# Performance work log

Hardware: AMD Instinct MI355X
Metric: run time of the kernel (lower is better)

The kernel has to match this reference:

```python
import jax, jax.numpy as jnp
import numpy as np

H = 1024
E = 8
TOP_K = 2
B, S = 4, 2048


def setup_inputs() -> dict:
    key = jax.random.key(0)
    ks = jax.random.split(key, 8)
    scale = 0.02
    return {
        "x": jax.random.normal(ks[0], (B, S, H), dtype=jnp.float32),
        "router_w": jax.random.normal(ks[1], (H, E), dtype=jnp.float32) * scale,
        "router_b": jnp.zeros((E,), dtype=jnp.float32),
        "w1": jax.random.normal(ks[2], (E, H, 4 * H), dtype=jnp.float32) * scale,
        "b1": jnp.zeros((E, 4 * H), dtype=jnp.float32),
        "w2": jax.random.normal(ks[3], (E, 4 * H, H), dtype=jnp.float32) * scale,
        "b2": jnp.zeros((E, H), dtype=jnp.float32),
    }


def reference(x, router_w, router_b, w1, b1, w2, b2):
    b, s, h = x.shape
    n_exp = w1.shape[0]
    x_flat = x.reshape(-1, h)  # [T, H]
    T = x_flat.shape[0]

    # Router: softmax then top-k, renormalize top-k probs (matches torch code).
    logits = x_flat @ router_w + router_b            # [T, E]
    probs = jax.nn.softmax(logits, axis=-1)
    top_values, top_indices = jax.lax.top_k(probs, TOP_K)  # [T, k]
    top_values = top_values / jnp.sum(top_values, axis=-1, keepdims=True)

    # Per-token combine weight for each expert (0 if token not routed there).
    combine = jnp.zeros((T, n_exp), dtype=x.dtype)
    combine = combine.at[jnp.arange(T)[:, None], top_indices].add(top_values)  # [T, E]

    # Loop over the small fixed expert set; masked combine weights zero out
    # contributions from unrouted tokens, matching the gather/scatter original.
    out = jnp.zeros_like(x_flat)
    for e in range(n_exp):
        hmid = jax.nn.gelu(x_flat @ w1[e] + b1[e], approximate=False)  # [T, 4H]
        y = hmid @ w2[e] + b2[e]                                       # [T, H]
        out = out + combine[:, e:e + 1] * y
    return out.reshape(b, s, h)
```

## Files before the change

kernel.cpp:

```cpp
#include <hip/hip_runtime.h>
#include <hip/hip_bf16.h>
#include <math.h>

#define TT 8192
#define HD 1024
#define FHD 4096
#define NE 8
#define NTMAX 136

typedef short s16x8 __attribute__((ext_vector_type(8)));
typedef float f32x4 __attribute__((ext_vector_type(4)));
using bf16 = __hip_bfloat16;
typedef unsigned int u32;

#define OFF_COUNTS 0
#define OFF_CURSOR 64
#define OFF_OFFS   128
#define OFF_E0     256
#define OFF_E1     (OFF_E0 + 4*TT)
#define OFF_W0     (OFF_E1 + 4*TT)
#define OFF_W1     (OFF_W0 + 4*TT)
#define OFF_S0     (OFF_W1 + 4*TT)
#define OFF_S1     (OFF_S0 + 4*TT)
#define OFF_TID    (OFF_S1 + 4*TT)
#define OFF_TW     (OFF_TID + 8*TT)
#define OFF_TMR    (OFF_TW + 8*TT)
#define OFF_TME    (OFF_TMR + 4*144)
#define OFF_TMN    (OFF_TME + 4*144)
#define OFF_XBF    (OFF_TMN + 64)
#define OFF_W1T    (OFF_XBF + 2*TT*HD)
#define OFF_W2T    (OFF_W1T + 2*NE*HD*FHD)
#define OFF_HMID   (OFF_W2T + 2*NE*HD*FHD)
#define OFF_YS     (OFF_HMID + (size_t)2*(2*TT)*FHD)

#define BM 128
#define BN 128
#define BK 32

__device__ __forceinline__ void gload_lds16(const void* g, void* l) {
    __builtin_amdgcn_global_load_lds(
        (const __attribute__((address_space(1))) u32*)g,
        (__attribute__((address_space(3))) u32*)l, 16, 0, 0);
}

__global__ __launch_bounds__(256) void cast_x_kernel(const float* __restrict__ x, bf16* __restrict__ xbf) {
    int i = (blockIdx.x * 256 + threadIdx.x) * 8;
    float4 a = *reinterpret_cast<const float4*>(&x[i]);
    float4 b = *reinterpret_cast<const float4*>(&x[i + 4]);
    bf16 h[8];
    h[0] = __float2bfloat16(a.x); h[1] = __float2bfloat16(a.y);
    h[2] = __float2bfloat16(a.z); h[3] = __float2bfloat16(a.w);
    h[4] = __float2bfloat16(b.x); h[5] = __float2bfloat16(b.y);
    h[6] = __float2bfloat16(b.z); h[7] = __float2bfloat16(b.w);
    *reinterpret_cast<uint4*>(&xbf[i]) = *reinterpret_cast<uint4*>(h);
}

__global__ __launch_bounds__(256) void transpose_cast_kernel(const float* __restrict__ in,
        bf16* __restrict__ out, int R, int C) {
    __shared__ float tile[64][65];
    int rt = R >> 6, ct = C >> 6;
    int e = blockIdx.x / (rt * ct);
    int rem = blockIdx.x % (rt * ct);
    int r0 = (rem / ct) << 6, c0 = (rem % ct) << 6;
    const float* ine = in + (size_t)e * R * C;
    bf16* oute = out + (size_t)e * R * C;
    int tid = threadIdx.x;
#pragma unroll
    for (int i = 0; i < 4; ++i) {
        int lin = tid + i * 256;
        int r = lin >> 4, cg = lin & 15;
        float4 v = *reinterpret_cast<const float4*>(&ine[(size_t)(r0 + r) * C + c0 + cg * 4]);
        tile[r][cg * 4 + 0] = v.x; tile[r][cg * 4 + 1] = v.y;
        tile[r][cg * 4 + 2] = v.z; tile[r][cg * 4 + 3] = v.w;
    }
    __syncthreads();
#pragma unroll
    for (int i = 0; i < 4; ++i) {
        int lin = tid + i * 256;
        int n = lin >> 4, kg = lin & 15;
        bf16 h[4];
        h[0] = __float2bfloat16(tile[kg * 4 + 0][n]);
        h[1] = __float2bfloat16(tile[kg * 4 + 1][n]);
        h[2] = __float2bfloat16(tile[kg * 4 + 2][n]);
        h[3] = __float2bfloat16(tile[kg * 4 + 3][n]);
        *reinterpret_cast<uint2*>(&oute[(size_t)(c0 + n) * R + r0 + kg * 4]) =
            *reinterpret_cast<uint2*>(h);
    }
}

__global__ __launch_bounds__(256) void router_kernel(const float* __restrict__ x,
        const float* __restrict__ rw, const float* __restrict__ rb,
        int* __restrict__ e0a, int* __restrict__ e1a,
        float* __restrict__ w0a, float* __restrict__ w1a, int* __restrict__ counts) {
    int wid = threadIdx.x >> 6, lane = threadIdx.x & 63;
    int t = blockIdx.x * 4 + wid;
    const float* xp = x + (size_t)t * HD + lane * 16;
    float xv[16];
#pragma unroll
    for (int j = 0; j < 4; ++j) {
        float4 v = *reinterpret_cast<const float4*>(&xp[j * 4]);
        xv[4 * j] = v.x; xv[4 * j + 1] = v.y; xv[4 * j + 2] = v.z; xv[4 * j + 3] = v.w;
    }
    float acc[8] = {0.f, 0.f, 0.f, 0.f, 0.f, 0.f, 0.f, 0.f};
    const float* rp = rw + (size_t)(lane * 16) * NE;
#pragma unroll
    for (int hh = 0; hh < 16; ++hh) {
        float4 r0 = *reinterpret_cast<const float4*>(&rp[hh * 8]);
        float4 r1 = *reinterpret_cast<const float4*>(&rp[hh * 8 + 4]);
        acc[0] += xv[hh] * r0.x; acc[1] += xv[hh] * r0.y;
        acc[2] += xv[hh] * r0.z; acc[3] += xv[hh] * r0.w;
        acc[4] += xv[hh] * r1.x; acc[5] += xv[hh] * r1.y;
        acc[6] += xv[hh] * r1.z; acc[7] += xv[hh] * r1.w;
    }
#pragma unroll
    for (int e = 0; e < 8; ++e) {
#pragma unroll
        for (int off = 32; off > 0; off >>= 1) acc[e] += __shfl_xor(acc[e], off, 64);
    }
    if (lane == 0) {
        float lg[8];
#pragma unroll
        for (int e = 0; e < 8; ++e) lg[e] = acc[e] + rb[e];
        int a = 0;
#pragma unroll
        for (int e = 1; e < 8; ++e) if (lg[e] > lg[a]) a = e;
        int b = (a == 0) ? 1 : 0;
#pragma unroll
        for (int e = 0; e < 8; ++e) if (e != a && e != b && lg[e] > lg[b]) b = e;
        float wa = 1.0f / (1.0f + expf(lg[b] - lg[a]));
        float wb = 1.0f / (1.0f + expf(lg[a] - lg[b]));
        e0a[t] = a; e1a[t] = b; w0a[t] = wa; w1a[t] = wb;
        atomicAdd(&counts[a], 1);
        atomicAdd(&counts[b], 1);
    }
}

__global__ void scan_offsets_kernel(const int* __restrict__ counts, int* __restrict__ offs,
        int* __restrict__ cursor, int* __restrict__ tmr, int* __restrict__ tme,
        int* __restrict__ tmn) {
    if (threadIdx.x == 0 && blockIdx.x == 0) {
        int s = 0, nt = 0;
        for (int e = 0; e < NE; ++e) {
            offs[e] = s; cursor[e] = s;
            int c = counts[e];
            for (int j = 0; j < c; j += BM) { tmr[nt] = s + j; tme[nt] = e; ++nt; }
            s += c;
        }
        offs[NE] = s;
        tmn[0] = nt;
        for (int i = nt; i < NTMAX; ++i) { tmr[i] = 0; tme[i] = 0; }
    }
}

__global__ __launch_bounds__(256) void scatter_kernel(const int* __restrict__ e0a, const int* __restrict__ e1a,
        const float* __restrict__ w0a, const float* __restrict__ w1a,
        int* __restrict__ cursor, int* __restrict__ tid_arr, float* __restrict__ tw_arr,
        int* __restrict__ slot0, int* __restrict__ slot1) {
    int t = blockIdx.x * 256 + threadIdx.x;
    int s0 = atomicAdd(&cursor[e0a[t]], 1);
    tid_arr[s0] = t; tw_arr[s0] = w0a[t]; slot0[t] = s0;
    int s1 = atomicAdd(&cursor[e1a[t]], 1);
    tid_arr[s1] = t; tw_arr[s1] = w1a[t]; slot1[t] = s1;
}

__global__ __launch_bounds__(256) void gemm1_kernel(const bf16* __restrict__ xbf, const bf16* __restrict__ w1t,
        const float* __restrict__ b1, const int* __restrict__ offs,
        const int* __restrict__ tid_arr, bf16* __restrict__ hmid,
        const int* __restrict__ tmr, const int* __restrict__ tme, const int* __restrict__ tmn) {
    __shared__ bf16 As[BM * BK];
    __shared__ bf16 Bs[BN * BK];
    __shared__ int toks[BM];
    int nwg = gridDim.x;
    int orig = blockIdx.x;
    int wg = (orig & 7) * (nwg >> 3) + (orig >> 3);
    int nt = wg / NTMAX;
    int tidx = wg % NTMAX;
    if (tidx >= tmn[0]) return;
    int e = tme[tidx];
    int row0 = tmr[tidx];
    int s1 = offs[e + 1];
    int n0 = nt * BN;
    int tid = threadIdx.x;
    if (tid < BM) { int s = row0 + tid; toks[tid] = tid_arr[(s < s1) ? s : (s1 - 1)]; }
    __syncthreads();
    int lane = tid & 63, w = tid >> 6;
    int wrow = (w >> 1) * 64, wcol = (w & 1) * 64;
    int lr = lane & 15, lk = (lane >> 4) * 8;
    int srow = lane >> 2, seg = lane & 3;
    int tokA0 = toks[w * 32 + srow];
    int tokA1 = toks[w * 32 + 16 + srow];
    const bf16* w1e = w1t + (size_t)e * FHD * HD;
    const bf16* bsrc0 = w1e + (size_t)(n0 + w * 32 + srow) * HD + seg * 8;
    const bf16* bsrc1 = w1e + (size_t)(n0 + w * 32 + 16 + srow) * HD + seg * 8;
    const bf16* asrc0 = xbf + (size_t)tokA0 * HD + seg * 8;
    const bf16* asrc1 = xbf + (size_t)tokA1 * HD + seg * 8;
    bf16* aDst0 = &As[(w * 32) * BK];
    bf16* aDst1 = &As[(w * 32 + 16) * BK];
    bf16* bDst0 = &Bs[(w * 32) * BK];
    bf16* bDst1 = &Bs[(w * 32 + 16) * BK];
    f32x4 acc[4][4] = {};
    for (int k0 = 0; k0 < HD; k0 += BK) {
        gload_lds16(asrc0 + k0, aDst0);
        gload_lds16(asrc1 + k0, aDst1);
        gload_lds16(bsrc0 + k0, bDst0);
        gload_lds16(bsrc1 + k0, bDst1);
        __syncthreads();
        s16x8 aF[4], bF[4];
#pragma unroll
        for (int m = 0; m < 4; ++m) aF[m] = *reinterpret_cast<const s16x8*>(&As[(wrow + m * 16 + lr) * BK + lk]);
#pragma unroll
        for (int n = 0; n < 4; ++n) bF[n] = *reinterpret_cast<const s16x8*>(&Bs[(wcol + n * 16 + lr) * BK + lk]);
#pragma unroll
        for (int m = 0; m < 4; ++m)
#pragma unroll
            for (int n = 0; n < 4; ++n)
                acc[m][n] = __builtin_amdgcn_mfma_f32_16x16x32_bf16(aF[m], bF[n], acc[m][n], 0, 0, 0);
        __syncthreads();
    }
#pragma unroll
    for (int m = 0; m < 4; ++m) {
#pragma unroll
        for (int n = 0; n < 4; ++n) {
            int col = n0 + wcol + n * 16 + lr;
            float bv = b1[(size_t)e * FHD + col];
#pragma unroll
            for (int r = 0; r < 4; ++r) {
                int row = wrow + m * 16 + (lane >> 4) * 4 + r;
                int slot = row0 + row;
                if (slot < s1) {
                    float v2 = acc[m][n][r] + bv;
                    v2 = 0.5f * v2 * (1.0f + erff(v2 * 0.70710678118f));
                    hmid[(size_t)slot * FHD + col] = __float2bfloat16(v2);
                }
            }
        }
    }
}

__global__ __launch_bounds__(256) void gemm2_kernel(const bf16* __restrict__ hmid, const bf16* __restrict__ w2t,
        const float* __restrict__ b2, const int* __restrict__ offs, float* __restrict__ ys,
        const int* __restrict__ tmr, const int* __restrict__ tme, const int* __restrict__ tmn) {
    __shared__ bf16 As[BM * BK];
    __shared__ bf16 Bs[BN * BK];
    int nwg = gridDim.x;
    int orig = blockIdx.x;
    int wg = (orig & 7) * (nwg >> 3) + (orig >> 3);
    int nt = wg / NTMAX;
    int tidx = wg % NTMAX;
    if (tidx >= tmn[0]) return;
    int e = tme[tidx];
    int row0 = tmr[tidx];
    int s1 = offs[e + 1];
    int n0 = nt * BN;
    int tid = threadIdx.x;
    int lane = tid & 63, w = tid >> 6;
    int wrow = (w >> 1) * 64, wcol = (w & 1) * 64;
    int lr = lane & 15, lk = (lane >> 4) * 8;
    int srow = lane >> 2, seg = lane & 3;
    int ar0 = row0 + w * 32 + srow;      if (ar0 >= s1) ar0 = s1 - 1;
    int ar1 = row0 + w * 32 + 16 + srow; if (ar1 >= s1) ar1 = s1 - 1;
    const bf16* w2e = w2t + (size_t)e * HD * FHD;
    const bf16* bsrc0 = w2e + (size_t)(n0 + w * 32 + srow) * FHD + seg * 8;
    const bf16* bsrc1 = w2e + (size_t)(n0 + w * 32 + 16 + srow) * FHD + seg * 8;
    const bf16* asrc0 = hmid + (size_t)ar0 * FHD + seg * 8;
    const bf16* asrc1 = hmid + (size_t)ar1 * FHD + seg * 8;
    bf16* aDst0 = &As[(w * 32) * BK];
    bf16* aDst1 = &As[(w * 32 + 16) * BK];
    bf16* bDst0 = &Bs[(w * 32) * BK];
    bf16* bDst1 = &Bs[(w * 32 + 16) * BK];
    f32x4 acc[4][4] = {};
    for (int k0 = 0; k0 < FHD; k0 += BK) {
        gload_lds16(asrc0 + k0, aDst0);
        gload_lds16(asrc1 + k0, aDst1);
        gload_lds16(bsrc0 + k0, bDst0);
        gload_lds16(bsrc1 + k0, bDst1);
        __syncthreads();
        s16x8 aF[4], bF[4];
#pragma unroll
        for (int m = 0; m < 4; ++m) aF[m] = *reinterpret_cast<const s16x8*>(&As[(wrow + m * 16 + lr) * BK + lk]);
#pragma unroll
        for (int n = 0; n < 4; ++n) bF[n] = *reinterpret_cast<const s16x8*>(&Bs[(wcol + n * 16 + lr) * BK + lk]);
#pragma unroll
        for (int m = 0; m < 4; ++m)
#pragma unroll
            for (int n = 0; n < 4; ++n)
                acc[m][n] = __builtin_amdgcn_mfma_f32_16x16x32_bf16(aF[m], bF[n], acc[m][n], 0, 0, 0);
        __syncthreads();
    }
#pragma unroll
    for (int m = 0; m < 4; ++m) {
#pragma unroll
        for (int n = 0; n < 4; ++n) {
            int col = n0 + wcol + n * 16 + lr;
            float bv = b2[(size_t)e * HD + col];
#pragma unroll
            for (int r = 0; r < 4; ++r) {
                int row = wrow + m * 16 + (lane >> 4) * 4 + r;
                int slot = row0 + row;
                if (slot < s1) ys[(size_t)slot * HD + col] = acc[m][n][r] + bv;
            }
        }
    }
}

__global__ __launch_bounds__(256) void combine_kernel(const float* __restrict__ ys,
        const int* __restrict__ slot0, const int* __restrict__ slot1,
        const float* __restrict__ tw, float* __restrict__ out) {
    int t = blockIdx.x;
    int c = threadIdx.x * 4;
    int sa = slot0[t], sb = slot1[t];
    float wa = tw[sa], wb = tw[sb];
    float4 a = *reinterpret_cast<const float4*>(&ys[(size_t)sa * HD + c]);
    float4 b = *reinterpret_cast<const float4*>(&ys[(size_t)sb * HD + c]);
    float4 o;
    o.x = wa * a.x + wb * b.x; o.y = wa * a.y + wb * b.y;
    o.z = wa * a.z + wb * b.z; o.w = wa * a.w + wb * b.w;
    *reinterpret_cast<float4*>(&out[(size_t)t * HD + c]) = o;
}

extern "C" void kernel_launch(void* const* d_in, const int* in_sizes, int n_in,
                              void* d_out, int out_size, void* d_ws, size_t ws_size,
                              hipStream_t stream) {
    const float* x  = (const float*)d_in[0];
    const float* rw = (const float*)d_in[1];
    const float* rb = (const float*)d_in[2];
    const float* w1 = (const float*)d_in[3];
    const float* b1 = (const float*)d_in[4];
    const float* w2 = (const float*)d_in[5];
    const float* b2 = (const float*)d_in[6];
    float* out = (float*)d_out;
    char* ws = (char*)d_ws;

    int*   counts  = (int*)(ws + OFF_COUNTS);
    int*   cursor  = (int*)(ws + OFF_CURSOR);
    int*   offs    = (int*)(ws + OFF_OFFS);
    int*   e0a     = (int*)(ws + OFF_E0);
    int*   e1a     = (int*)(ws + OFF_E1);
    float* w0a     = (float*)(ws + OFF_W0);
    float* w1a     = (float*)(ws + OFF_W1);
    int*   slot0   = (int*)(ws + OFF_S0);
    int*   slot1   = (int*)(ws + OFF_S1);
    int*   tid_arr = (int*)(ws + OFF_TID);
    float* tw_arr  = (float*)(ws + OFF_TW);
    int*   tmr     = (int*)(ws + OFF_TMR);
    int*   tme     = (int*)(ws + OFF_TME);
    int*   tmn     = (int*)(ws + OFF_TMN);
    bf16*  xbf     = (bf16*)(ws + OFF_XBF);
    bf16*  w1t     = (bf16*)(ws + OFF_W1T);
    bf16*  w2t     = (bf16*)(ws + OFF_W2T);
    bf16*  hmid    = (bf16*)(ws + OFF_HMID);
    float* ys      = (float*)(ws + OFF_YS);

    hipMemsetAsync(counts, 0, 64, stream);

    cast_x_kernel<<<TT * HD / 2048, 256, 0, stream>>>(x, xbf);
    transpose_cast_kernel<<<NE * (HD / 64) * (FHD / 64), 256, 0, stream>>>(w1, w1t, HD, FHD);
    transpose_cast_kernel<<<NE * (FHD / 64) * (HD / 64), 256, 0, stream>>>(w2, w2t, FHD, HD);
    router_kernel<<<TT / 4, 256, 0, stream>>>(x, rw, rb, e0a, e1a, w0a, w1a, counts);
    scan_offsets_kernel<<<1, 64, 0, stream>>>(counts, offs, cursor, tmr, tme, tmn);
    scatter_kernel<<<TT / 256, 256, 0, stream>>>(e0a, e1a, w0a, w1a, cursor, tid_arr, tw_arr, slot0, slot1);
    gemm1_kernel<<<(FHD / BN) * NTMAX, 256, 0, stream>>>(xbf, w1t, b1, offs, tid_arr, hmid, tmr, tme, tmn);
    gemm2_kernel<<<(HD / BN) * NTMAX, 256, 0, stream>>>(hmid, w2t, b2, offs, ys, tmr, tme, tmn);
    combine_kernel<<<TT, 256, 0, stream>>>(ys, slot0, slot1, tw_arr, out);
}
```

Before: 929.2 us.

## Fuse weight transpose, x cast, router and offset scan into one prep kernel

Merges the x cast, both weight transpose-casts, the router, and the offset/tile-map scan into a single prep kernel. The x bf16 cast is folded into the router's existing x read, and the last router block (found with a done-counter atomic) builds offsets and the tile map in parallel. The aim is to remove several kernel launches and a redundant read of x. The BM/BN/BK macros are also inlined as literals. The done counter sits inside the 64-byte region that is memset each call, so it is reset correctly. The fused scan relies on threadfence and atomic ordering.

```diff
diff --git a/kernel.cpp b/kernel.cpp
--- a/kernel.cpp
+++ b/kernel.cpp
@@ -14,6 +14,7 @@
 typedef unsigned int u32;
 
 #define OFF_COUNTS 0
+#define OFF_DONE   32
 #define OFF_CURSOR 64
 #define OFF_OFFS   128
 #define OFF_E0     256
@@ -33,73 +34,74 @@
 #define OFF_HMID   (OFF_W2T + 2*NE*HD*FHD)
 #define OFF_YS     (OFF_HMID + (size_t)2*(2*TT)*FHD)
 
-#define BM 128
-#define BN 128
-#define BK 32
-
 __device__ __forceinline__ void gload_lds16(const void* g, void* l) {
     __builtin_amdgcn_global_load_lds(
         (const __attribute__((address_space(1))) u32*)g,
         (__attribute__((address_space(3))) u32*)l, 16, 0, 0);
 }
 
-__global__ __launch_bounds__(256) void cast_x_kernel(const float* __restrict__ x, bf16* __restrict__ xbf) {
-    int i = (blockIdx.x * 256 + threadIdx.x) * 8;
-    float4 a = *reinterpret_cast<const float4*>(&x[i]);
-    float4 b = *reinterpret_cast<const float4*>(&x[i + 4]);
-    bf16 h[8];
-    h[0] = __float2bfloat16(a.x); h[1] = __float2bfloat16(a.y);
-    h[2] = __float2bfloat16(a.z); h[3] = __float2bfloat16(a.w);
-    h[4] = __float2bfloat16(b.x); h[5] = __float2bfloat16(b.y);
-    h[6] = __float2bfloat16(b.z); h[7] = __float2bfloat16(b.w);
-    *reinterpret_cast<uint4*>(&xbf[i]) = *reinterpret_cast<uint4*>(h);
-}
-
-__global__ __launch_bounds__(256) void transpose_cast_kernel(const float* __restrict__ in,
-        bf16* __restrict__ out, int R, int C) {
+__global__ __launch_bounds__(256) void prep_kernel(
+        const float* __restrict__ x, const float* __restrict__ rw, const float* __restrict__ rb,
+        const float* __restrict__ w1, const float* __restrict__ w2,
+        bf16* __restrict__ xbf, bf16* __restrict__ w1t, bf16* __restrict__ w2t,
+        int* __restrict__ e0a, int* __restrict__ e1a,
+        float* __restrict__ w0a, float* __restrict__ w1a,
+        int* __restrict__ counts, int* __restrict__ done,
+        int* __restrict__ offs, int* __restrict__ cursor,
+        int* __restrict__ tmr, int* __restrict__ tme, int* __restrict__ tmn) {
     __shared__ float tile[64][65];
-    int rt = R >> 6, ct = C >> 6;
-    int e = blockIdx.x / (rt * ct);
-    int rem = blockIdx.x % (rt * ct);
-    int r0 = (rem / ct) << 6, c0 = (rem % ct) << 6;
-    const float* ine = in + (size_t)e * R * C;
-    bf16* oute = out + (size_t)e * R * C;
+    int bid = blockIdx.x;
     int tid = threadIdx.x;
-#pragma unroll
-    for (int i = 0; i < 4; ++i) {
-        int lin = tid + i * 256;
-        int r = lin >> 4, cg = lin & 15;
-        float4 v = *reinterpret_cast<const float4*>(&ine[(size_t)(r0 + r) * C + c0 + cg * 4]);
-        tile[r][cg * 4 + 0] = v.x; tile[r][cg * 4 + 1] = v.y;
-        tile[r][cg * 4 + 2] = v.z; tile[r][cg * 4 + 3] = v.w;
-    }
-    __syncthreads();
-#pragma unroll
-    for (int i = 0; i < 4; ++i) {
-        int lin = tid + i * 256;
-        int n = lin >> 4, kg = lin & 15;
-        bf16 h[4];
-        h[0] = __float2bfloat16(tile[kg * 4 + 0][n]);
-        h[1] = __float2bfloat16(tile[kg * 4 + 1][n]);
-        h[2] = __float2bfloat16(tile[kg * 4 + 2][n]);
-        h[3] = __float2bfloat16(tile[kg * 4 + 3][n]);
-        *reinterpret_cast<uint2*>(&oute[(size_t)(c0 + n) * R + r0 + kg * 4]) =
-            *reinterpret_cast<uint2*>(h);
-    }
-}
-
-__global__ __launch_bounds__(256) void router_kernel(const float* __restrict__ x,
-        const float* __restrict__ rw, const float* __restrict__ rb,
-        int* __restrict__ e0a, int* __restrict__ e1a,
-        float* __restrict__ w0a, float* __restrict__ w1a, int* __restrict__ counts) {
-    int wid = threadIdx.x >> 6, lane = threadIdx.x & 63;
-    int t = blockIdx.x * 4 + wid;
+    if (bid < 16384) {
+        const float* in; bf16* out; int R, C, rem;
+        if (bid < 8192) { in = w1; out = w1t; R = HD;  C = FHD; rem = bid; }
+        else            { in = w2; out = w2t; R = FHD; C = HD;  rem = bid - 8192; }
+        int rt = R >> 6, ct = C >> 6;
+        int e = rem / (rt * ct);
+        int rem2 = rem % (rt * ct);
+        int r0 = (rem2 / ct) << 6, c0 = (rem2 % ct) << 6;
+        const float* ine = in + (size_t)e * R * C;
+        bf16* oute = out + (size_t)e * R * C;
+#pragma unroll
+        for (int i = 0; i < 4; ++i) {
+            int lin = tid + i * 256;
+            int r = lin >> 4, cg = lin & 15;
+            float4 v = *reinterpret_cast<const float4*>(&ine[(size_t)(r0 + r) * C + c0 + cg * 4]);
+            tile[r][cg * 4 + 0] = v.x; tile[r][cg * 4 + 1] = v.y;
+            tile[r][cg * 4 + 2] = v.z; tile[r][cg * 4 + 3] = v.w;
+        }
+        __syncthreads();
+#pragma unroll
+        for (int i = 0; i < 4; ++i) {
+            int lin = tid + i * 256;
+            int n = lin >> 4, kg = lin & 15;
+            bf16 h[4];
+            h[0] = __float2bfloat16(tile[kg * 4 + 0][n]);
+            h[1] = __float2bfloat16(tile[kg * 4 + 1][n]);
+            h[2] = __float2bfloat16(tile[kg * 4 + 2][n]);
+            h[3] = __float2bfloat16(tile[kg * 4 + 3][n]);
+            *reinterpret_cast<uint2*>(&oute[(size_t)(c0 + n) * R + r0 + kg * 4]) =
+                *reinterpret_cast<uint2*>(h);
+        }
+        return;
+    }
+    int rbid = bid - 16384;
+    int wid = tid >> 6, lane = tid & 63;
+    int t = rbid * 4 + wid;
     const float* xp = x + (size_t)t * HD + lane * 16;
     float xv[16];
 #pragma unroll
     for (int j = 0; j < 4; ++j) {
         float4 v = *reinterpret_cast<const float4*>(&xp[j * 4]);
         xv[4 * j] = v.x; xv[4 * j + 1] = v.y; xv[4 * j + 2] = v.z; xv[4 * j + 3] = v.w;
+    }
+    {
+        bf16 hv[16];
+#pragma unroll
+        for (int j = 0; j < 16; ++j) hv[j] = __float2bfloat16(xv[j]);
+        uint4* dst = reinterpret_cast<uint4*>(&xbf[(size_t)t * HD + lane * 16]);
+        dst[0] = reinterpret_cast<uint4*>(hv)[0];
+        dst[1] = reinterpret_cast<uint4*>(hv)[1];
     }
     float acc[8] = {0.f, 0.f, 0.f, 0.f, 0.f, 0.f, 0.f, 0.f};
     const float* rp = rw + (size_t)(lane * 16) * NE;
@@ -133,22 +135,37 @@
         atomicAdd(&counts[a], 1);
         atomicAdd(&counts[b], 1);
     }
-}
-
-__global__ void scan_offsets_kernel(const int* __restrict__ counts, int* __restrict__ offs,
-        int* __restrict__ cursor, int* __restrict__ tmr, int* __restrict__ tme,
-        int* __restrict__ tmn) {
-    if (threadIdx.x == 0 && blockIdx.x == 0) {
-        int s = 0, nt = 0;
+    __syncthreads();
+    __shared__ int lastFlag;
+    if (tid == 0) {
+        __threadfence();
+        lastFlag = (atomicAdd(done, 1) == 2047) ? 1 : 0;
+    }
+    __syncthreads();
+    if (!lastFlag) return;
+    __threadfence();
+    __shared__ int cbase[NE + 1], tbase[NE + 1];
+    if (tid == 0) {
+        int s = 0, ntt = 0;
         for (int e = 0; e < NE; ++e) {
-            offs[e] = s; cursor[e] = s;
-            int c = counts[e];
-            for (int j = 0; j < c; j += BM) { tmr[nt] = s + j; tme[nt] = e; ++nt; }
-            s += c;
-        }
+            int c = atomicAdd(&counts[e], 0);
+            cbase[e] = s; tbase[e] = ntt;
+            s += c; ntt += (c + 127) >> 7;
+        }
+        cbase[NE] = s; tbase[NE] = ntt;
+        tmn[0] = ntt;
         offs[NE] = s;
-        tmn[0] = nt;
-        for (int i = nt; i < NTMAX; ++i) { tmr[i] = 0; tme[i] = 0; }
+    }
+    __syncthreads();
+    if (tid < NE) { offs[tid] = cbase[tid]; cursor[tid] = cbase[tid]; }
+    if (tid < NTMAX) {
+        int ntt = tbase[NE];
+        if (tid < ntt) {
+            int e = 0;
+            while (tbase[e + 1] <= tid) ++e;
+            tmr[tid] = cbase[e] + ((tid - tbase[e]) << 7);
+            tme[tid] = e;
+        } else { tmr[tid] = 0; tme[tid] = 0; }
     }
 }
 
@@ -167,9 +184,9 @@
         const float* __restrict__ b1, const int* __restrict__ offs,
         const int* __restrict__ tid_arr, bf16* __restrict__ hmid,
         const int* __restrict__ tmr, const int* __restrict__ tme, const int* __restrict__ tmn) {
-    __shared__ bf16 As[BM * BK];
-    __shared__ bf16 Bs[BN * BK];
-    __shared__ int toks[BM];
+    __shared__ bf16 As[128 * 32];
+    __shared__ bf16 Bs[128 * 32];
+    __shared__ int toks[128];
     int nwg = gridDim.x;
     int orig = blockIdx.x;
     int wg = (orig & 7) * (nwg >> 3) + (orig >> 3);
@@ -179,9 +196,9 @@
     int e = tme[tidx];
     int row0 = tmr[tidx];
     int s1 = offs[e + 1];
-    int n0 = nt * BN;
+    int n0 = nt * 128;
     int tid = threadIdx.x;
-    if (tid < BM) { int s = row0 + tid; toks[tid] = tid_arr[(s < s1) ? s : (s1 - 1)]; }
+    if (tid < 128) { int s = row0 + tid; toks[tid] = tid_arr[(s < s1) ? s : (s1 - 1)]; }
     __syncthreads();
     int lane = tid & 63, w = tid >> 6;
     int wrow = (w >> 1) * 64, wcol = (w & 1) * 64;
@@ -194,12 +211,12 @@
     const bf16* bsrc1 = w1e + (size_t)(n0 + w * 32 + 16 + srow) * HD + seg * 8;
     const bf16* asrc0 = xbf + (size_t)tokA0 * HD + seg * 8;
     const bf16* asrc1 = xbf + (size_t)tokA1 * HD + seg * 8;
-    bf16* aDst0 = &As[(w * 32) * BK];
-    bf16* aDst1 = &As[(w * 32 + 16) * BK];
-    bf16* bDst0 = &Bs[(w * 32) * BK];
-    bf16* bDst1 = &Bs[(w * 32 + 16) * BK];
+    bf16* aDst0 = &As[(w * 32) * 32];
+    bf16* aDst1 = &As[(w * 32 + 16) * 32];
+    bf16* bDst0 = &Bs[(w * 32) * 32];
+    bf16* bDst1 = &Bs[(w * 32 + 16) * 32];
     f32x4 acc[4][4] = {};
-    for (int k0 = 0; k0 < HD; k0 += BK) {
+    for (int k0 = 0; k0 < HD; k0 += 32) {
         gload_lds16(asrc0 + k0, aDst0);
         gload_lds16(asrc1 + k0, aDst1);
         gload_lds16(bsrc0 + k0, bDst0);
@@ -207,9 +224,9 @@
         __syncthreads();
         s16x8 aF[4], bF[4];
 #pragma unroll
-        for (int m = 0; m < 4; ++m) aF[m] = *reinterpret_cast<const s16x8*>(&As[(wrow + m * 16 + lr) * BK + lk]);
-#pragma unroll
-        for (int n = 0; n < 4; ++n) bF[n] = *reinterpret_cast<const s16x8*>(&Bs[(wcol + n * 16 + lr) * BK + lk]);
+        for (int m = 0; m < 4; ++m) aF[m] = *reinterpret_cast<const s16x8*>(&As[(wrow + m * 16 + lr) * 32 + lk]);
+#pragma unroll
+        for (int n = 0; n < 4; ++n) bF[n] = *reinterpret_cast<const s16x8*>(&Bs[(wcol + n * 16 + lr) * 32 + lk]);
 #pragma unroll
         for (int m = 0; m < 4; ++m)
 #pragma unroll
@@ -240,8 +257,8 @@
 __global__ __launch_bounds__(256) void gemm2_kernel(const bf16* __restrict__ hmid, const bf16* __restrict__ w2t,
         const float* __restrict__ b2, const int* __restrict__ offs, float* __restrict__ ys,
         const int* __restrict__ tmr, const int* __restrict__ tme, const int* __restrict__ tmn) {
-    __shared__ bf16 As[BM * BK];
-    __shared__ bf16 Bs[BN * BK];
+    __shared__ bf16 As[128 * 32];
+    __shared__ bf16 Bs[128 * 32];
     int nwg = gridDim.x;
     int orig = blockIdx.x;
     int wg = (orig & 7) * (nwg >> 3) + (orig >> 3);
@@ -251,7 +268,7 @@
     int e = tme[tidx];
     int row0 = tmr[tidx];
     int s1 = offs[e + 1];
-    int n0 = nt * BN;
+    int n0 = nt * 128;
     int tid = threadIdx.x;
     int lane = tid & 63, w = tid >> 6;
     int wrow = (w >> 1) * 64, wcol = (w & 1) * 64;
@@ -264,12 +281,12 @@
     const bf16* bsrc1 = w2e + (size_t)(n0 + w * 32 + 16 + srow) * FHD + seg * 8;
     const bf16* asrc0 = hmid + (size_t)ar0 * FHD + seg * 8;
     const bf16* asrc1 = hmid + (size_t)ar1 * FHD + seg * 8;
-    bf16* aDst0 = &As[(w * 32) * BK];
-    bf16* aDst1 = &As[(w * 32 + 16) * BK];
-    bf16* bDst0 = &Bs[(w * 32) * BK];
-    bf16* bDst1 = &Bs[(w * 32 + 16) * BK];
+    bf16* aDst0 = &As[(w * 32) * 32];
+    bf16* aDst1 = &As[(w * 32 + 16) * 32];
+    bf16* bDst0 = &Bs[(w * 32) * 32];
+    bf16* bDst1 = &Bs[(w * 32 + 16) * 32];
     f32x4 acc[4][4] = {};
-    for (int k0 = 0; k0 < FHD; k0 += BK) {
+    for (int k0 = 0; k0 < FHD; k0 += 32) {
         gload_lds16(asrc0 + k0, aDst0);
         gload_lds16(asrc1 + k0, aDst1);
         gload_lds16(bsrc0 + k0, bDst0);
@@ -277,9 +294,9 @@
         __syncthreads();
         s16x8 aF[4], bF[4];
 #pragma unroll
-        for (int m = 0; m < 4; ++m) aF[m] = *reinterpret_cast<const s16x8*>(&As[(wrow + m * 16 + lr) * BK + lk]);
-#pragma unroll
-        for (int n = 0; n < 4; ++n) bF[n] = *reinterpret_cast<const s16x8*>(&Bs[(wcol + n * 16 + lr) * BK + lk]);
+        for (int m = 0; m < 4; ++m) aF[m] = *reinterpret_cast<const s16x8*>(&As[(wrow + m * 16 + lr) * 32 + lk]);
+#pragma unroll
+        for (int n = 0; n < 4; ++n) bF[n] = *reinterpret_cast<const s16x8*>(&Bs[(wcol + n * 16 + lr) * 32 + lk]);
 #pragma unroll
         for (int m = 0; m < 4; ++m)
 #pragma unroll
@@ -332,6 +349,7 @@
     char* ws = (char*)d_ws;
 
     int*   counts  = (int*)(ws + OFF_COUNTS);
+    int*   done    = (int*)(ws + OFF_DONE);
     int*   cursor  = (int*)(ws + OFF_CURSOR);
     int*   offs    = (int*)(ws + OFF_OFFS);
     int*   e0a     = (int*)(ws + OFF_E0);
@@ -353,13 +371,11 @@
 
     hipMemsetAsync(counts, 0, 64, stream);
 
-    cast_x_kernel<<<TT * HD / 2048, 256, 0, stream>>>(x, xbf);
-    transpose_cast_kernel<<<NE * (HD / 64) * (FHD / 64), 256, 0, stream>>>(w1, w1t, HD, FHD);
-    transpose_cast_kernel<<<NE * (FHD / 64) * (HD / 64), 256, 0, stream>>>(w2, w2t, FHD, HD);
-    router_kernel<<<TT / 4, 256, 0, stream>>>(x, rw, rb, e0a, e1a, w0a, w1a, counts);
-    scan_offsets_kernel<<<1, 64, 0, stream>>>(counts, offs, cursor, tmr, tme, tmn);
-    scatter_kernel<<<TT / 256, 256, 0, stream>>>(e0a, e1a, w0a, w1a, cursor, tid_arr, tw_arr, slot0, slot1);
-    gemm1_kernel<<<(FHD / BN) * NTMAX, 256, 0, stream>>>(xbf, w1t, b1, offs, tid_arr, hmid, tmr, tme, tmn);
-    gemm2_kernel<<<(HD / BN) * NTMAX, 256, 0, stream>>>(hmid, w2t, b2, offs, ys, tmr, tme, tmn);
+    prep_kernel<<<18432, 256, 0, stream>>>(x, rw, rb, w1, w2, xbf, w1t, w2t,
+        e0a, e1a, w0a, w1a, counts, done, offs, cursor, tmr, tme, tmn);
+    scatter_kernel<<<TT / 256, 256, 0, stream>>>(e0a, e1a, w0a, w1a, cursor,
+        tid_arr, tw_arr, slot0, slot1);
+    gemm1_kernel<<<(FHD / 128) * NTMAX, 256, 0, stream>>>(xbf, w1t, b1, offs, tid_arr, hmid, tmr, tme, tmn);
+    gemm2_kernel<<<(HD / 128) * NTMAX, 256, 0, stream>>>(hmid, w2t, b2, offs, ys, tmr, tme, tmn);
     combine_kernel<<<TT, 256, 0, stream>>>(ys, slot0, slot1, tw_arr, out);
 }
```

Result: no change. 921.7 us (-0.8%).
